# Kernel optimization log

Measured on AMD Instinct MI355X. Metric: run time of the kernel, lower is better.

The kernel has to match this reference:

```python
import jax, jax.numpy as jnp
import numpy as np

N, E, D, B, C = 50000, 800000, 128, 20000, 40
EPS_BN = 1e-3    # keras BatchNormalization default epsilon
EPS_NRM = 1e-12  # keras ops.nn.normalize epsilon
FFN_DIMS = {"pre": (D, D), "c1p": (D, D), "c1u": (2 * D, D), "c2p": (D, D), "c2u": (2 * D, D), "post": (D, D)}


def setup_inputs() -> dict:
    key = jax.random.key(0)
    ks = jax.random.split(key, 8)
    inp = {
        "node_features": jax.random.normal(ks[0], (N, D), jnp.float32),
        "edges": jax.random.randint(ks[1], (2, E), 0, N, dtype=jnp.int32),
        "edge_w": jax.random.uniform(ks[2], (E,), jnp.float32),
        "input_node_idx": jax.random.randint(ks[3], (B,), 0, N, dtype=jnp.int32),
    }
    for i, (name, (din, dout)) in enumerate(FFN_DIMS.items()):
        kw = jax.random.fold_in(key, 100 + i)
        inp[name + "_g"] = jnp.ones((din,), jnp.float32)
        inp[name + "_be"] = jnp.zeros((din,), jnp.float32)
        inp[name + "_mu"] = jnp.zeros((din,), jnp.float32)
        inp[name + "_var"] = jnp.ones((din,), jnp.float32)
        inp[name + "_w"] = jax.random.normal(kw, (din, dout), jnp.float32) * (1.0 / float(np.sqrt(din)))
        inp[name + "_bi"] = jnp.zeros((dout,), jnp.float32)
    inp["logits_w"] = jax.random.normal(ks[4], (D, C), jnp.float32) * (1.0 / float(np.sqrt(D)))
    inp["logits_b"] = jnp.zeros((C,), jnp.float32)
    return inp


def ffn(x, g, be, mu, var, w, bi):
    # BatchNorm (inference running stats) -> Dropout (identity) -> Dense + exact gelu
    xn = (x - mu) * jax.lax.rsqrt(var + EPS_BN) * g + be
    return jax.nn.gelu(xn @ w + bi, approximate=False)


def l2norm(x):
    n = jnp.sqrt(jnp.sum(x * x, axis=-1, keepdims=True))
    return x / jnp.maximum(n, EPS_NRM)


def graph_conv(x, node_idx, nbr_idx, ew, prep, upd):
    # gather neighbours -> prepare FFN -> edge-weighted -> segment_sum (reduce='sum')
    msgs = ffn(x[nbr_idx], *prep) * ew[:, None]                         # [E, D]
    red = jax.ops.segment_sum(msgs, node_idx, num_segments=x.shape[0])  # [N, D]
    h = jnp.concatenate([x, red], axis=1)                               # [N, 2D] (combination='concat')
    return l2norm(ffn(h, *upd))                                         # normalize=True


def reference(node_features, edges, edge_w, input_node_idx,
              pre_g, pre_be, pre_mu, pre_var, pre_w, pre_bi,
              c1p_g, c1p_be, c1p_mu, c1p_var, c1p_w, c1p_bi,
              c1u_g, c1u_be, c1u_mu, c1u_var, c1u_w, c1u_bi,
              c2p_g, c2p_be, c2p_mu, c2p_var, c2p_w, c2p_bi,
              c2u_g, c2u_be, c2u_mu, c2u_var, c2u_w, c2u_bi,
              post_g, post_be, post_mu, post_var, post_w, post_bi,
              logits_w, logits_b):
    ew = edge_w / jnp.sum(edge_w)                       # edge_W normalized at init
    node_idx, nbr_idx = edges[0], edges[1]
    x = ffn(node_features, pre_g, pre_be, pre_mu, pre_var, pre_w, pre_bi)
    x = graph_conv(x, node_idx, nbr_idx, ew,
                   (c1p_g, c1p_be, c1p_mu, c1p_var, c1p_w, c1p_bi),
                   (c1u_g, c1u_be, c1u_mu, c1u_var, c1u_w, c1u_bi)) + x
    x = graph_conv(x, node_idx, nbr_idx, ew,
                   (c2p_g, c2p_be, c2p_mu, c2p_var, c2p_w, c2p_bi),
                   (c2u_g, c2u_be, c2u_mu, c2u_var, c2u_w, c2u_bi)) + x
    x = ffn(x, post_g, post_be, post_mu, post_var, post_w, post_bi)
    return x[input_node_idx] @ logits_w + logits_b      # [B, C]
```

## Files before the change

### kernel.cpp

```cpp
#include <hip/hip_runtime.h>
#include <hip/hip_fp16.h>
#include <math.h>

static constexpr int D = 128;
static constexpr int CAP = 64;
static constexpr float EPS_BN = 1e-3f;

typedef short short8 __attribute__((ext_vector_type(8)));
typedef short short4v __attribute__((ext_vector_type(4)));
typedef float float4v __attribute__((ext_vector_type(4)));

__device__ __forceinline__ float gelu_exact(float x) {
    return 0.5f * x * (1.0f + erff(x * 0.70710678118654752f));
}

__device__ __forceinline__ void f32_to_hilo(float f, short& h, short& l) {
    unsigned u = __float_as_uint(f);
    h = (short)(u >> 16);
    float hf = __uint_as_float(u & 0xFFFF0000u);
    unsigned lu = __float_as_uint(f - hf);
    l = (short)(lu >> 16);
}

__device__ __forceinline__ short f32_to_bf16_rne(float f) {
    unsigned u = __float_as_uint(f);
    u += 0x7FFFu + ((u >> 16) & 1u);
    return (short)(u >> 16);
}

struct FoldArgs {
    const float* g[6]; const float* be[6]; const float* mu[6];
    const float* var[6]; const float* w[6]; const float* bi[6];
    short* wh[6]; short* wl[6]; float* bp[6]; int K[6];
};

__global__ void k_build(const int* __restrict__ edges, const float* __restrict__ ew,
                        int* __restrict__ cnt, float* __restrict__ sums,
                        unsigned* __restrict__ cw, FoldArgs fa, int E, int N, int fillBlocks) {
    __shared__ float sm[4];
    const int tid = threadIdx.x;
    const int lane = tid & 63, wvi = tid >> 6;

    if ((int)blockIdx.x < fillBlocks) {
        const int g = blockIdx.x & 7;
        const int bid = blockIdx.x >> 3;
        const int gstride = (fillBlocks >> 3) * 256;
        const int N8 = (N + 7) >> 3;
        const int lo = g * N8;
        const int hi = min(lo + N8, N);
        float s = 0.f;
        for (int e = bid * 256 + tid; e < E; e += gstride) {
            int dst = edges[e];
            if (dst >= lo && dst < hi) {
                int src = edges[E + e];
                float w = ew[e];
                s += w;
                unsigned short wb = __half_as_ushort(__float2half(w));
                int idx = atomicAdd(&cnt[dst], 1);
                if (idx < CAP)
                    cw[(size_t)dst * CAP + idx] = ((unsigned)src << 16) | (unsigned)wb;
            }
        }
        for (int off = 32; off > 0; off >>= 1) s += __shfl_down(s, off, 64);
        if (lane == 0) sm[wvi] = s;
        __syncthreads();
        if (tid == 0) {
            float t = sm[0] + sm[1] + sm[2] + sm[3];
            if (t != 0.f) atomicAdd(sums, t);
        }
    } else {
        const int idx = blockIdx.x - fillBlocks;
        const int f = idx >> 7;
        const int c = idx & 127;
        const int K = fa.K[f];
        const float* g = fa.g[f]; const float* be = fa.be[f];
        const float* mu = fa.mu[f]; const float* var = fa.var[f];
        const float* w = fa.w[f]; const float* bi = fa.bi[f];
        short* wh = fa.wh[f]; short* wl = fa.wl[f]; float* bp = fa.bp[f];
        float part = 0.f;
        for (int k = tid; k < K; k += blockDim.x) {
            float a = g[k] / sqrtf(var[k] + EPS_BN);
            float wv = w[k * D + c];
            float prod = a * wv;
            short hh, ll;
            f32_to_hilo(prod, hh, ll);
            wh[c * K + k] = hh;
            wl[c * K + k] = ll;
            part += (be[k] - mu[k] * a) * wv;
        }
        for (int off = 32; off > 0; off >>= 1) part += __shfl_down(part, off, 64);
        if (lane == 0) sm[wvi] = part;
        __syncthreads();
        if (tid == 0) bp[c] = bi[c] + sm[0] + sm[1] + sm[2] + sm[3];
    }
}

__global__ void k_reduce(const int* __restrict__ cnt, const unsigned* __restrict__ cw,
                         const float* __restrict__ sums, const __half* __restrict__ y,
                         float* __restrict__ red, int N) {
    int n = blockIdx.x * (blockDim.x >> 6) + (threadIdx.x >> 6);
    if (n >= N) return;
    float inv = 1.0f / sums[0];
    int lane = threadIdx.x & 63;
    int sub = lane >> 4;
    int q = lane & 15;
    int count = min(cnt[n], CAP);
    int start = n * CAP;
    int end = start + count;
    float acc[8] = {0.f, 0.f, 0.f, 0.f, 0.f, 0.f, 0.f, 0.f};
    int i = start + sub;
    if (i < end) {
        unsigned c = cw[i];
        for (;;) {
            int ni = i + 4;
            unsigned nc = 0;
            if (ni < end) nc = cw[ni];
            int src = (int)(c >> 16);
            float w = __half2float(__ushort_as_half((unsigned short)(c & 0xFFFFu))) * inv;
            float4 raw = *((const float4*)(y + (size_t)src * D) + q);
            const __half2* hp = (const __half2*)&raw;
            #pragma unroll
            for (int t = 0; t < 4; t++) {
                float2 f = __half22float2(hp[t]);
                acc[t * 2]     += w * f.x;
                acc[t * 2 + 1] += w * f.y;
            }
            if (ni >= end) break;
            i = ni; c = nc;
        }
    }
    #pragma unroll
    for (int t = 0; t < 8; t++) {
        acc[t] += __shfl_xor(acc[t], 16, 64);
        acc[t] += __shfl_xor(acc[t], 32, 64);
    }
    if (sub == 0) {
        float4 o0 = {acc[0], acc[1], acc[2], acc[3]};
        float4 o1 = {acc[4], acc[5], acc[6], acc[7]};
        *((float4*)(red + (size_t)n * D + q * 8)) = o0;
        *((float4*)(red + (size_t)n * D + q * 8 + 4)) = o1;
    }
}

template<int K, bool L2RES, bool OUT16, bool SPLIT3>
__device__ __forceinline__ void ffn_body(
    short (*__restrict__ Abuf)[128][72], short (*__restrict__ Wbuf)[128][72],
    float (*__restrict__ rs)[2],
    const float* __restrict__ A0, const float* __restrict__ A1,
    const short* __restrict__ Wh, const short* __restrict__ Wl,
    const float* __restrict__ bp, const float* __restrict__ resid,
    float* __restrict__ outf, __half* __restrict__ outh, int nrows)
{
    const int tid = threadIdx.x;
    const int lane = tid & 63;
    const int wv = tid >> 6;
    const int wr = wv >> 1;
    const int wc = wv & 1;
    const int m = lane & 15;
    const int quad = lane >> 4;
    const int rowBlock = blockIdx.x * 128;

    float4v acc[4][4];
    #pragma unroll
    for (int ti = 0; ti < 4; ti++)
        #pragma unroll
        for (int tj = 0; tj < 4; tj++)
            acc[ti][tj] = (float4v){0.f, 0.f, 0.f, 0.f};

    for (int cc = 0; cc < K / 64; cc++) {
        const float* Asrc = (K == 256 && cc >= 2) ? A1 : A0;
        const int kb = (K == 256) ? ((cc & 1) * 64) : (cc * 64);
        const int kw = cc * 64;

        #pragma unroll
        for (int t = 0; t < 8; t++) {
            int i = tid + t * 256;
            int r = i >> 4, k4 = i & 15;
            int grow = rowBlock + r; if (grow >= nrows) grow = nrows - 1;
            float4 f = *((const float4*)(Asrc + (size_t)grow * D + kb) + k4);
            if (SPLIT3) {
                short h0, l0, h1, l1, h2, l2, h3, l3;
                f32_to_hilo(f.x, h0, l0);
                f32_to_hilo(f.y, h1, l1);
                f32_to_hilo(f.z, h2, l2);
                f32_to_hilo(f.w, h3, l3);
                short4v hh = {h0, h1, h2, h3};
                short4v ll = {l0, l1, l2, l3};
                *(short4v*)&Abuf[0][r][k4 * 4] = hh;
                *(short4v*)&Abuf[1][r][k4 * 4] = ll;
            } else {
                short4v hh = {f32_to_bf16_rne(f.x), f32_to_bf16_rne(f.y),
                              f32_to_bf16_rne(f.z), f32_to_bf16_rne(f.w)};
                *(short4v*)&Abuf[0][r][k4 * 4] = hh;
            }
        }
        #pragma unroll
        for (int t = 0; t < 4; t++) {
            int i = tid + t * 256;
            int c = i >> 3, g = i & 7;
            short8 wh8 = *(const short8*)(Wh + (size_t)c * K + kw + g * 8);
            *(short8*)&Wbuf[0][c][g * 8] = wh8;
            if (SPLIT3) {
                short8 wl8 = *(const short8*)(Wl + (size_t)c * K + kw + g * 8);
                *(short8*)&Wbuf[1][c][g * 8] = wl8;
            }
        }
        __syncthreads();

        #pragma unroll
        for (int ks = 0; ks < 2; ks++) {
            short8 ah[4], bh[4];
            #pragma unroll
            for (int ti = 0; ti < 4; ti++)
                ah[ti] = *(const short8*)&Abuf[0][wr * 64 + ti * 16 + m][ks * 32 + quad * 8];
            #pragma unroll
            for (int tj = 0; tj < 4; tj++)
                bh[tj] = *(const short8*)&Wbuf[0][wc * 64 + tj * 16 + m][ks * 32 + quad * 8];
            if (SPLIT3) {
                short8 al[4], bl[4];
                #pragma unroll
                for (int ti = 0; ti < 4; ti++)
                    al[ti] = *(const short8*)&Abuf[1][wr * 64 + ti * 16 + m][ks * 32 + quad * 8];
                #pragma unroll
                for (int tj = 0; tj < 4; tj++)
                    bl[tj] = *(const short8*)&Wbuf[1][wc * 64 + tj * 16 + m][ks * 32 + quad * 8];
                #pragma unroll
                for (int ti = 0; ti < 4; ti++)
                    #pragma unroll
                    for (int tj = 0; tj < 4; tj++) {
                        acc[ti][tj] = __builtin_amdgcn_mfma_f32_16x16x32_bf16(al[ti], bh[tj], acc[ti][tj], 0, 0, 0);
                        acc[ti][tj] = __builtin_amdgcn_mfma_f32_16x16x32_bf16(ah[ti], bl[tj], acc[ti][tj], 0, 0, 0);
                        acc[ti][tj] = __builtin_amdgcn_mfma_f32_16x16x32_bf16(ah[ti], bh[tj], acc[ti][tj], 0, 0, 0);
                    }
            } else {
                #pragma unroll
                for (int ti = 0; ti < 4; ti++)
                    #pragma unroll
                    for (int tj = 0; tj < 4; tj++)
                        acc[ti][tj] = __builtin_amdgcn_mfma_f32_16x16x32_bf16(ah[ti], bh[tj], acc[ti][tj], 0, 0, 0);
            }
        }
        __syncthreads();
    }

    float bvv[4];
    #pragma unroll
    for (int tj = 0; tj < 4; tj++) bvv[tj] = bp[wc * 64 + tj * 16 + m];

    float g[4][4][4];
    #pragma unroll
    for (int ti = 0; ti < 4; ti++)
        #pragma unroll
        for (int tj = 0; tj < 4; tj++)
            #pragma unroll
            for (int r4 = 0; r4 < 4; r4++)
                g[ti][tj][r4] = gelu_exact(acc[ti][tj][r4] + bvv[tj]);

    if (L2RES) {
        #pragma unroll
        for (int ti = 0; ti < 4; ti++)
            #pragma unroll
            for (int r4 = 0; r4 < 4; r4++) {
                float ss = 0.f;
                #pragma unroll
                for (int tj = 0; tj < 4; tj++) ss += g[ti][tj][r4] * g[ti][tj][r4];
                ss += __shfl_xor(ss, 1, 64);
                ss += __shfl_xor(ss, 2, 64);
                ss += __shfl_xor(ss, 4, 64);
                ss += __shfl_xor(ss, 8, 64);
                if (m == 0) rs[wr * 64 + ti * 16 + quad * 4 + r4][wc] = ss;
            }
        __syncthreads();
        #pragma unroll
        for (int ti = 0; ti < 4; ti++)
            #pragma unroll
            for (int r4 = 0; r4 < 4; r4++) {
                int rib = wr * 64 + ti * 16 + quad * 4 + r4;
                float tot = rs[rib][0] + rs[rib][1];
                float inv = 1.0f / fmaxf(sqrtf(tot), 1e-12f);
                int row = rowBlock + rib;
                if (row < nrows) {
                    #pragma unroll
                    for (int tj = 0; tj < 4; tj++) {
                        int c = wc * 64 + tj * 16 + m;
                        outf[(size_t)row * D + c] = g[ti][tj][r4] * inv + resid[(size_t)row * D + c];
                    }
                }
            }
    } else {
        #pragma unroll
        for (int ti = 0; ti < 4; ti++)
            #pragma unroll
            for (int r4 = 0; r4 < 4; r4++) {
                int row = rowBlock + wr * 64 + ti * 16 + quad * 4 + r4;
                if (row < nrows) {
                    #pragma unroll
                    for (int tj = 0; tj < 4; tj++) {
                        int c = wc * 64 + tj * 16 + m;
                        if (OUT16) outh[(size_t)row * D + c] = __float2half(g[ti][tj][r4]);
                        else       outf[(size_t)row * D + c] = g[ti][tj][r4];
                    }
                }
            }
    }
}

__global__ __launch_bounds__(256, 2) void k_pair1(
    const float* __restrict__ nf,
    const short* __restrict__ Wh0, const short* __restrict__ Wl0, const float* __restrict__ Bp0,
    float* __restrict__ xA,
    const short* __restrict__ Wh1, const float* __restrict__ Bp1,
    __half* __restrict__ yh, int N)
{
    __shared__ short Abuf[2][128][72];
    __shared__ short Wbuf[2][128][72];
    __shared__ float rs[128][2];
    ffn_body<128, false, false, true>(Abuf, Wbuf, rs, nf, nullptr, Wh0, Wl0, Bp0, nullptr, xA, nullptr, N);
    __syncthreads();
    ffn_body<128, false, true, false>(Abuf, Wbuf, rs, xA, nullptr, Wh1, nullptr, Bp1, nullptr, nullptr, yh, N);
}

__global__ __launch_bounds__(256, 2) void k_pair2(
    const float* __restrict__ xA, const float* __restrict__ red,
    const short* __restrict__ Wh2, const short* __restrict__ Wl2, const float* __restrict__ Bp2,
    float* __restrict__ y,
    const short* __restrict__ Wh3, const float* __restrict__ Bp3,
    __half* __restrict__ yh, int N)
{
    __shared__ short Abuf[2][128][72];
    __shared__ short Wbuf[2][128][72];
    __shared__ float rs[128][2];
    ffn_body<256, true, false, true>(Abuf, Wbuf, rs, xA, red, Wh2, Wl2, Bp2, xA, y, nullptr, N);
    __syncthreads();
    ffn_body<128, false, true, false>(Abuf, Wbuf, rs, y, nullptr, Wh3, nullptr, Bp3, nullptr, nullptr, yh, N);
}

__global__ __launch_bounds__(256, 2) void k_pair3(
    const float* __restrict__ y, const float* __restrict__ red_in,
    const short* __restrict__ Wh4, const short* __restrict__ Wl4, const float* __restrict__ Bp4,
    float* __restrict__ xA,
    const short* __restrict__ Wh5, const short* __restrict__ Wl5, const float* __restrict__ Bp5,
    float* __restrict__ yout, int N)
{
    __shared__ short Abuf[2][128][72];
    __shared__ short Wbuf[2][128][72];
    __shared__ float rs[128][2];
    ffn_body<256, true, false, true>(Abuf, Wbuf, rs, y, red_in, Wh4, Wl4, Bp4, y, xA, nullptr, N);
    __syncthreads();
    ffn_body<128, false, false, true>(Abuf, Wbuf, rs, xA, nullptr, Wh5, Wl5, Bp5, nullptr, yout, nullptr, N);
}

__global__ void k_logits(const float* __restrict__ x, const int* __restrict__ idx,
                         const float* __restrict__ LW, const float* __restrict__ lb,
                         float* __restrict__ out, int B) {
    int wid = blockIdx.x * 4 + (threadIdx.x >> 6);
    int lane = threadIdx.x & 63;
    if (wid >= B) return;
    int row = __builtin_amdgcn_readfirstlane(idx[wid]);
    if (lane >= 40) return;
    float acc = lb[lane];
    const float4* xr = (const float4*)(x + (size_t)row * D);
    #pragma unroll 4
    for (int k4 = 0; k4 < 32; k4++) {
        float4 xv = xr[k4];
        acc += xv.x * LW[(4 * k4 + 0) * 40 + lane];
        acc += xv.y * LW[(4 * k4 + 1) * 40 + lane];
        acc += xv.z * LW[(4 * k4 + 2) * 40 + lane];
        acc += xv.w * LW[(4 * k4 + 3) * 40 + lane];
    }
    out[(size_t)wid * 40 + lane] = acc;
}

extern "C" void kernel_launch(void* const* d_in, const int* in_sizes, int n_in,
                              void* d_out, int out_size, void* d_ws, size_t ws_size,
                              hipStream_t stream) {
    const float* node_features = (const float*)d_in[0];
    const int*   edges         = (const int*)d_in[1];
    const float* edge_w        = (const float*)d_in[2];
    const int*   input_idx     = (const int*)d_in[3];
    const int N = in_sizes[0] / D;
    const int E = in_sizes[2];
    const int B = in_sizes[3];

    const float* P[6][6];
    for (int f = 0; f < 6; f++)
        for (int q = 0; q < 6; q++)
            P[f][q] = (const float*)d_in[4 + f * 6 + q];
    const float* logits_w = (const float*)d_in[40];
    const float* logits_b = (const float*)d_in[41];

    float* ws = (float*)d_ws;
    size_t nd = (size_t)N * D;
    float* xA  = ws;
    float* y   = ws + nd;
    float* red = ws + 2 * nd;
    float* p   = ws + 3 * nd;
    __half* yh = (__half*)p; p += nd / 2;
    const int Ks[6] = {128, 128, 256, 128, 256, 128};
    short* Wh[6]; short* Wl[6]; float* Bp[6];
    {
        short* sp = (short*)p;
        for (int f = 0; f < 6; f++) {
            Wh[f] = sp; sp += (size_t)Ks[f] * D;
            Wl[f] = sp; sp += (size_t)Ks[f] * D;
        }
        p = (float*)sp;
    }
    for (int f = 0; f < 6; f++) { Bp[f] = p; p += D; }
    int* cnt    = (int*)p; p += N;
    float* sums = p; p += 2;
    unsigned* cw = (unsigned*)p; p += (size_t)N * CAP;

    FoldArgs fa;
    for (int f = 0; f < 6; f++) {
        fa.g[f] = P[f][0]; fa.be[f] = P[f][1]; fa.mu[f] = P[f][2];
        fa.var[f] = P[f][3]; fa.w[f] = P[f][4]; fa.bi[f] = P[f][5];
        fa.wh[f] = Wh[f]; fa.wl[f] = Wl[f]; fa.bp[f] = Bp[f]; fa.K[f] = Ks[f];
    }

    const int fillBlocks = 1024;
    hipMemsetAsync(cnt, 0, ((size_t)N + 2) * sizeof(int), stream);
    k_build<<<fillBlocks + 768, 256, 0, stream>>>(edges, edge_w, cnt, sums, cw, fa, E, N, fillBlocks);

    const int gb = (N + 127) / 128;
    const int rb = (N + 3) / 4;

    k_pair1<<<gb, 256, 0, stream>>>(node_features, Wh[0], Wl[0], Bp[0], xA, Wh[1], Bp[1], yh, N);
    k_reduce<<<rb, 256, 0, stream>>>(cnt, cw, sums, yh, red, N);
    k_pair2<<<gb, 256, 0, stream>>>(xA, red, Wh[2], Wl[2], Bp[2], y, Wh[3], Bp[3], yh, N);
    k_reduce<<<rb, 256, 0, stream>>>(cnt, cw, sums, yh, red, N);
    k_pair3<<<gb, 256, 0, stream>>>(y, red, Wh[4], Wl[4], Bp[4], xA, Wh[5], Wl[5], Bp[5], red, N);
    k_logits<<<(B + 3) / 4, 256, 0, stream>>>(red, input_idx, logits_w, logits_b, (float*)d_out, B);
}
```

Before: 411.8 us.

## Fuse edge-bucket build into first FFN pair, store reductions in fp16, drop weight LDS staging

```diff
diff --git a/kernel.cpp b/kernel.cpp
--- a/kernel.cpp
+++ b/kernel.cpp
@@ -34,17 +34,229 @@
     short* wh[6]; short* wl[6]; float* bp[6]; int K[6];
 };
 
-__global__ void k_build(const int* __restrict__ edges, const float* __restrict__ ew,
-                        int* __restrict__ cnt, float* __restrict__ sums,
-                        unsigned* __restrict__ cw, FoldArgs fa, int E, int N, int fillBlocks) {
+__global__ void k_fold_all(FoldArgs fa) {
+    const int f = blockIdx.y;
+    const int c = blockIdx.x;
+    const int K = fa.K[f];
+    const float* g = fa.g[f]; const float* be = fa.be[f];
+    const float* mu = fa.mu[f]; const float* var = fa.var[f];
+    const float* w = fa.w[f]; const float* bi = fa.bi[f];
+    short* wh = fa.wh[f]; short* wl = fa.wl[f]; float* bp = fa.bp[f];
+    float part = 0.f;
+    for (int k = threadIdx.x; k < K; k += blockDim.x) {
+        float a = g[k] / sqrtf(var[k] + EPS_BN);
+        float wv = w[k * D + c];
+        float prod = a * wv;
+        short hh, ll;
+        f32_to_hilo(prod, hh, ll);
+        wh[c * K + k] = hh;
+        wl[c * K + k] = ll;
+        part += (be[k] - mu[k] * a) * wv;
+    }
+    for (int off = 32; off > 0; off >>= 1) part += __shfl_down(part, off, 64);
     __shared__ float sm[4];
+    int lane = threadIdx.x & 63, wv_ = threadIdx.x >> 6;
+    if (lane == 0) sm[wv_] = part;
+    __syncthreads();
+    if (threadIdx.x == 0) bp[c] = bi[c] + sm[0] + sm[1] + sm[2] + sm[3];
+}
+
+template<int K, bool L2RES, bool OUT16, bool SPLIT3>
+__device__ __forceinline__ void ffn_body(
+    short (*__restrict__ Abuf)[128][72], float (*__restrict__ rs)[2],
+    int rowBlock,
+    const float* __restrict__ A0, const __half* __restrict__ A1,
+    const float* __restrict__ sums,
+    const short* __restrict__ Wh, const short* __restrict__ Wl,
+    const float* __restrict__ bp, const float* __restrict__ resid,
+    float* __restrict__ outf, __half* __restrict__ outh, int nrows)
+{
     const int tid = threadIdx.x;
-    const int lane = tid & 63, wvi = tid >> 6;
-
-    if ((int)blockIdx.x < fillBlocks) {
+    const int lane = tid & 63;
+    const int wv = tid >> 6;
+    const int wr = wv >> 1;
+    const int wc = wv & 1;
+    const int m = lane & 15;
+    const int quad = lane >> 4;
+
+    float inv = 1.0f;
+    if (K == 256) inv = 1.0f / sums[0];
+
+    float4v acc[4][4];
+    #pragma unroll
+    for (int ti = 0; ti < 4; ti++)
+        #pragma unroll
+        for (int tj = 0; tj < 4; tj++)
+            acc[ti][tj] = (float4v){0.f, 0.f, 0.f, 0.f};
+
+    for (int cc = 0; cc < K / 64; cc++) {
+        const int kb = (K == 256) ? ((cc & 1) * 64) : (cc * 64);
+        const int kw = cc * 64;
+        const bool useA1 = (K == 256 && cc >= 2);
+
+        if (!useA1) {
+            #pragma unroll
+            for (int t = 0; t < 8; t++) {
+                int i = tid + t * 256;
+                int r = i >> 4, k4 = i & 15;
+                int grow = rowBlock + r; if (grow >= nrows) grow = nrows - 1;
+                float4 f = *((const float4*)(A0 + (size_t)grow * D + kb) + k4);
+                if (SPLIT3) {
+                    short h0, l0, h1, l1, h2, l2, h3, l3;
+                    f32_to_hilo(f.x, h0, l0);
+                    f32_to_hilo(f.y, h1, l1);
+                    f32_to_hilo(f.z, h2, l2);
+                    f32_to_hilo(f.w, h3, l3);
+                    short4v hh = {h0, h1, h2, h3};
+                    short4v ll = {l0, l1, l2, l3};
+                    *(short4v*)&Abuf[0][r][k4 * 4] = hh;
+                    *(short4v*)&Abuf[1][r][k4 * 4] = ll;
+                } else {
+                    short4v hh = {f32_to_bf16_rne(f.x), f32_to_bf16_rne(f.y),
+                                  f32_to_bf16_rne(f.z), f32_to_bf16_rne(f.w)};
+                    *(short4v*)&Abuf[0][r][k4 * 4] = hh;
+                }
+            }
+        } else {
+            #pragma unroll
+            for (int t = 0; t < 4; t++) {
+                int i = tid + t * 256;
+                int r = i >> 3, g8 = i & 7;
+                int grow = rowBlock + r; if (grow >= nrows) grow = nrows - 1;
+                float4 raw = *((const float4*)(A1 + (size_t)grow * D + kb) + g8);
+                const __half2* hp = (const __half2*)&raw;
+                short hs[8], ls[8];
+                #pragma unroll
+                for (int j = 0; j < 4; j++) {
+                    float2 fv = __half22float2(hp[j]);
+                    f32_to_hilo(fv.x * inv, hs[2 * j], ls[2 * j]);
+                    f32_to_hilo(fv.y * inv, hs[2 * j + 1], ls[2 * j + 1]);
+                }
+                short8 hv = {hs[0], hs[1], hs[2], hs[3], hs[4], hs[5], hs[6], hs[7]};
+                short8 lv = {ls[0], ls[1], ls[2], ls[3], ls[4], ls[5], ls[6], ls[7]};
+                *(short8*)&Abuf[0][r][g8 * 8] = hv;
+                *(short8*)&Abuf[1][r][g8 * 8] = lv;
+            }
+        }
+        __syncthreads();
+
+        #pragma unroll
+        for (int ks = 0; ks < 2; ks++) {
+            short8 ah[4], bh[4];
+            #pragma unroll
+            for (int ti = 0; ti < 4; ti++)
+                ah[ti] = *(const short8*)&Abuf[0][wr * 64 + ti * 16 + m][ks * 32 + quad * 8];
+            #pragma unroll
+            for (int tj = 0; tj < 4; tj++)
+                bh[tj] = *(const short8*)(Wh + (size_t)(wc * 64 + tj * 16 + m) * K + kw + ks * 32 + quad * 8);
+            if (SPLIT3) {
+                short8 al[4], bl[4];
+                #pragma unroll
+                for (int ti = 0; ti < 4; ti++)
+                    al[ti] = *(const short8*)&Abuf[1][wr * 64 + ti * 16 + m][ks * 32 + quad * 8];
+                #pragma unroll
+                for (int tj = 0; tj < 4; tj++)
+                    bl[tj] = *(const short8*)(Wl + (size_t)(wc * 64 + tj * 16 + m) * K + kw + ks * 32 + quad * 8);
+                #pragma unroll
+                for (int ti = 0; ti < 4; ti++)
+                    #pragma unroll
+                    for (int tj = 0; tj < 4; tj++) {
+                        acc[ti][tj] = __builtin_amdgcn_mfma_f32_16x16x32_bf16(al[ti], bh[tj], acc[ti][tj], 0, 0, 0);
+                        acc[ti][tj] = __builtin_amdgcn_mfma_f32_16x16x32_bf16(ah[ti], bl[tj], acc[ti][tj], 0, 0, 0);
+                        acc[ti][tj] = __builtin_amdgcn_mfma_f32_16x16x32_bf16(ah[ti], bh[tj], acc[ti][tj], 0, 0, 0);
+                    }
+            } else {
+                #pragma unroll
+                for (int ti = 0; ti < 4; ti++)
+                    #pragma unroll
+                    for (int tj = 0; tj < 4; tj++)
+                        acc[ti][tj] = __builtin_amdgcn_mfma_f32_16x16x32_bf16(ah[ti], bh[tj], acc[ti][tj], 0, 0, 0);
+            }
+        }
+        __syncthreads();
+    }
+
+    float bvv[4];
+    #pragma unroll
+    for (int tj = 0; tj < 4; tj++) bvv[tj] = bp[wc * 64 + tj * 16 + m];
+
+    float g[4][4][4];
+    #pragma unroll
+    for (int ti = 0; ti < 4; ti++)
+        #pragma unroll
+        for (int tj = 0; tj < 4; tj++)
+            #pragma unroll
+            for (int r4 = 0; r4 < 4; r4++)
+                g[ti][tj][r4] = gelu_exact(acc[ti][tj][r4] + bvv[tj]);
+
+    if (L2RES) {
+        #pragma unroll
+        for (int ti = 0; ti < 4; ti++)
+            #pragma unroll
+            for (int r4 = 0; r4 < 4; r4++) {
+                float ss = 0.f;
+                #pragma unroll
+                for (int tj = 0; tj < 4; tj++) ss += g[ti][tj][r4] * g[ti][tj][r4];
+                ss += __shfl_xor(ss, 1, 64);
+                ss += __shfl_xor(ss, 2, 64);
+                ss += __shfl_xor(ss, 4, 64);
+                ss += __shfl_xor(ss, 8, 64);
+                if (m == 0) rs[wr * 64 + ti * 16 + quad * 4 + r4][wc] = ss;
+            }
+        __syncthreads();
+        #pragma unroll
+        for (int ti = 0; ti < 4; ti++)
+            #pragma unroll
+            for (int r4 = 0; r4 < 4; r4++) {
+                int rib = wr * 64 + ti * 16 + quad * 4 + r4;
+                float tot = rs[rib][0] + rs[rib][1];
+                float invn = 1.0f / fmaxf(sqrtf(tot), 1e-12f);
+                int row = rowBlock + rib;
+                if (row < nrows) {
+                    #pragma unroll
+                    for (int tj = 0; tj < 4; tj++) {
+                        int c = wc * 64 + tj * 16 + m;
+                        outf[(size_t)row * D + c] = g[ti][tj][r4] * invn + resid[(size_t)row * D + c];
+                    }
+                }
+            }
+    } else {
+        #pragma unroll
+        for (int ti = 0; ti < 4; ti++)
+            #pragma unroll
+            for (int r4 = 0; r4 < 4; r4++) {
+                int row = rowBlock + wr * 64 + ti * 16 + quad * 4 + r4;
+                if (row < nrows) {
+                    #pragma unroll
+                    for (int tj = 0; tj < 4; tj++) {
+                        int c = wc * 64 + tj * 16 + m;
+                        if (OUT16) outh[(size_t)row * D + c] = __float2half(g[ti][tj][r4]);
+                        else       outf[(size_t)row * D + c] = g[ti][tj][r4];
+                    }
+                }
+            }
+    }
+}
+
+__global__ __launch_bounds__(256, 3) void k_pair1f(
+    const int* __restrict__ edges, const float* __restrict__ ew,
+    int* __restrict__ cnt, float* __restrict__ sums, unsigned* __restrict__ cw,
+    const float* __restrict__ nf,
+    const short* __restrict__ Wh0, const short* __restrict__ Wl0, const float* __restrict__ Bp0,
+    float* __restrict__ xA,
+    const short* __restrict__ Wh1, const float* __restrict__ Bp1,
+    __half* __restrict__ yh, int E, int N, int FB)
+{
+    __shared__ short Abuf[2][128][72];
+    __shared__ float rs[128][2];
+    __shared__ float sm4[4];
+
+    if ((int)blockIdx.x < FB) {
+        const int tid = threadIdx.x;
+        const int lane = tid & 63, wvi = tid >> 6;
         const int g = blockIdx.x & 7;
         const int bid = blockIdx.x >> 3;
-        const int gstride = (fillBlocks >> 3) * 256;
+        const int gstride = (FB >> 3) * 256;
         const int N8 = (N + 7) >> 3;
         const int lo = g * N8;
         const int hi = min(lo + N8, N);
@@ -62,45 +274,55 @@
             }
         }
         for (int off = 32; off > 0; off >>= 1) s += __shfl_down(s, off, 64);
-        if (lane == 0) sm[wvi] = s;
+        if (lane == 0) sm4[wvi] = s;
         __syncthreads();
         if (tid == 0) {
-            float t = sm[0] + sm[1] + sm[2] + sm[3];
+            float t = sm4[0] + sm4[1] + sm4[2] + sm4[3];
             if (t != 0.f) atomicAdd(sums, t);
         }
-    } else {
-        const int idx = blockIdx.x - fillBlocks;
-        const int f = idx >> 7;
-        const int c = idx & 127;
-        const int K = fa.K[f];
-        const float* g = fa.g[f]; const float* be = fa.be[f];
-        const float* mu = fa.mu[f]; const float* var = fa.var[f];
-        const float* w = fa.w[f]; const float* bi = fa.bi[f];
-        short* wh = fa.wh[f]; short* wl = fa.wl[f]; float* bp = fa.bp[f];
-        float part = 0.f;
-        for (int k = tid; k < K; k += blockDim.x) {
-            float a = g[k] / sqrtf(var[k] + EPS_BN);
-            float wv = w[k * D + c];
-            float prod = a * wv;
-            short hh, ll;
-            f32_to_hilo(prod, hh, ll);
-            wh[c * K + k] = hh;
-            wl[c * K + k] = ll;
-            part += (be[k] - mu[k] * a) * wv;
-        }
-        for (int off = 32; off > 0; off >>= 1) part += __shfl_down(part, off, 64);
-        if (lane == 0) sm[wvi] = part;
-        __syncthreads();
-        if (tid == 0) bp[c] = bi[c] + sm[0] + sm[1] + sm[2] + sm[3];
-    }
+        return;
+    }
+
+    int rowBlock = ((int)blockIdx.x - FB) * 128;
+    ffn_body<128, false, false, true>(Abuf, rs, rowBlock, nf, nullptr, nullptr, Wh0, Wl0, Bp0, nullptr, xA, nullptr, N);
+    __syncthreads();
+    ffn_body<128, false, true, false>(Abuf, rs, rowBlock, xA, nullptr, nullptr, Wh1, nullptr, Bp1, nullptr, nullptr, yh, N);
+}
+
+__global__ __launch_bounds__(256, 3) void k_pair2(
+    const float* __restrict__ xA, const __half* __restrict__ red, const float* __restrict__ sums,
+    const short* __restrict__ Wh2, const short* __restrict__ Wl2, const float* __restrict__ Bp2,
+    float* __restrict__ y,
+    const short* __restrict__ Wh3, const float* __restrict__ Bp3,
+    __half* __restrict__ yh, int N)
+{
+    __shared__ short Abuf[2][128][72];
+    __shared__ float rs[128][2];
+    int rowBlock = blockIdx.x * 128;
+    ffn_body<256, true, false, true>(Abuf, rs, rowBlock, xA, red, sums, Wh2, Wl2, Bp2, xA, y, nullptr, N);
+    __syncthreads();
+    ffn_body<128, false, true, false>(Abuf, rs, rowBlock, y, nullptr, nullptr, Wh3, nullptr, Bp3, nullptr, nullptr, yh, N);
+}
+
+__global__ __launch_bounds__(256, 3) void k_pair3(
+    const float* __restrict__ y, const __half* __restrict__ red, const float* __restrict__ sums,
+    const short* __restrict__ Wh4, const short* __restrict__ Wl4, const float* __restrict__ Bp4,
+    float* __restrict__ xA,
+    const short* __restrict__ Wh5, const short* __restrict__ Wl5, const float* __restrict__ Bp5,
+    __half* __restrict__ yh, int N)
+{
+    __shared__ short Abuf[2][128][72];
+    __shared__ float rs[128][2];
+    int rowBlock = blockIdx.x * 128;
+    ffn_body<256, true, false, true>(Abuf, rs, rowBlock, y, red, sums, Wh4, Wl4, Bp4, y, xA, nullptr, N);
+    __syncthreads();
+    ffn_body<128, false, true, true>(Abuf, rs, rowBlock, xA, nullptr, nullptr, Wh5, Wl5, Bp5, nullptr, nullptr, yh, N);
 }
 
 __global__ void k_reduce(const int* __restrict__ cnt, const unsigned* __restrict__ cw,
-                         const float* __restrict__ sums, const __half* __restrict__ y,
-                         float* __restrict__ red, int N) {
+                         const __half* __restrict__ y, __half* __restrict__ red, int N) {
     int n = blockIdx.x * (blockDim.x >> 6) + (threadIdx.x >> 6);
     if (n >= N) return;
-    float inv = 1.0f / sums[0];
     int lane = threadIdx.x & 63;
     int sub = lane >> 4;
     int q = lane & 15;
@@ -116,7 +338,7 @@
             unsigned nc = 0;
             if (ni < end) nc = cw[ni];
             int src = (int)(c >> 16);
-            float w = __half2float(__ushort_as_half((unsigned short)(c & 0xFFFFu))) * inv;
+            float w = __half2float(__ushort_as_half((unsigned short)(c & 0xFFFFu)));
             float4 raw = *((const float4*)(y + (size_t)src * D) + q);
             const __half2* hp = (const __half2*)&raw;
             #pragma unroll
@@ -135,222 +357,16 @@
         acc[t] += __shfl_xor(acc[t], 32, 64);
     }
     if (sub == 0) {
-        float4 o0 = {acc[0], acc[1], acc[2], acc[3]};
-        float4 o1 = {acc[4], acc[5], acc[6], acc[7]};
-        *((float4*)(red + (size_t)n * D + q * 8)) = o0;
-        *((float4*)(red + (size_t)n * D + q * 8 + 4)) = o1;
-    }
-}
-
-template<int K, bool L2RES, bool OUT16, bool SPLIT3>
-__device__ __forceinline__ void ffn_body(
-    short (*__restrict__ Abuf)[128][72], short (*__restrict__ Wbuf)[128][72],
-    float (*__restrict__ rs)[2],
-    const float* __restrict__ A0, const float* __restrict__ A1,
-    const short* __restrict__ Wh, const short* __restrict__ Wl,
-    const float* __restrict__ bp, const float* __restrict__ resid,
-    float* __restrict__ outf, __half* __restrict__ outh, int nrows)
-{
-    const int tid = threadIdx.x;
-    const int lane = tid & 63;
-    const int wv = tid >> 6;
-    const int wr = wv >> 1;
-    const int wc = wv & 1;
-    const int m = lane & 15;
-    const int quad = lane >> 4;
-    const int rowBlock = blockIdx.x * 128;
-
-    float4v acc[4][4];
-    #pragma unroll
-    for (int ti = 0; ti < 4; ti++)
-        #pragma unroll
-        for (int tj = 0; tj < 4; tj++)
-            acc[ti][tj] = (float4v){0.f, 0.f, 0.f, 0.f};
-
-    for (int cc = 0; cc < K / 64; cc++) {
-        const float* Asrc = (K == 256 && cc >= 2) ? A1 : A0;
-        const int kb = (K == 256) ? ((cc & 1) * 64) : (cc * 64);
-        const int kw = cc * 64;
-
-        #pragma unroll
-        for (int t = 0; t < 8; t++) {
-            int i = tid + t * 256;
-            int r = i >> 4, k4 = i & 15;
-            int grow = rowBlock + r; if (grow >= nrows) grow = nrows - 1;
-            float4 f = *((const float4*)(Asrc + (size_t)grow * D + kb) + k4);
-            if (SPLIT3) {
-                short h0, l0, h1, l1, h2, l2, h3, l3;
-                f32_to_hilo(f.x, h0, l0);
-                f32_to_hilo(f.y, h1, l1);
-                f32_to_hilo(f.z, h2, l2);
-                f32_to_hilo(f.w, h3, l3);
-                short4v hh = {h0, h1, h2, h3};
-                short4v ll = {l0, l1, l2, l3};
-                *(short4v*)&Abuf[0][r][k4 * 4] = hh;
-                *(short4v*)&Abuf[1][r][k4 * 4] = ll;
-            } else {
-                short4v hh = {f32_to_bf16_rne(f.x), f32_to_bf16_rne(f.y),
-                              f32_to_bf16_rne(f.z), f32_to_bf16_rne(f.w)};
-                *(short4v*)&Abuf[0][r][k4 * 4] = hh;
-            }
-        }
-        #pragma unroll
-        for (int t = 0; t < 4; t++) {
-            int i = tid + t * 256;
-            int c = i >> 3, g = i & 7;
-            short8 wh8 = *(const short8*)(Wh + (size_t)c * K + kw + g * 8);
-            *(short8*)&Wbuf[0][c][g * 8] = wh8;
-            if (SPLIT3) {
-                short8 wl8 = *(const short8*)(Wl + (size_t)c * K + kw + g * 8);
-                *(short8*)&Wbuf[1][c][g * 8] = wl8;
-            }
-        }
-        __syncthreads();
-
-        #pragma unroll
-        for (int ks = 0; ks < 2; ks++) {
-            short8 ah[4], bh[4];
-            #pragma unroll
-            for (int ti = 0; ti < 4; ti++)
-                ah[ti] = *(const short8*)&Abuf[0][wr * 64 + ti * 16 + m][ks * 32 + quad * 8];
-            #pragma unroll
-            for (int tj = 0; tj < 4; tj++)
-                bh[tj] = *(const short8*)&Wbuf[0][wc * 64 + tj * 16 + m][ks * 32 + quad * 8];
-            if (SPLIT3) {
-                short8 al[4], bl[4];
-                #pragma unroll
-                for (int ti = 0; ti < 4; ti++)
-                    al[ti] = *(const short8*)&Abuf[1][wr * 64 + ti * 16 + m][ks * 32 + quad * 8];
-                #pragma unroll
-                for (int tj = 0; tj < 4; tj++)
-                    bl[tj] = *(const short8*)&Wbuf[1][wc * 64 + tj * 16 + m][ks * 32 + quad * 8];
-                #pragma unroll
-                for (int ti = 0; ti < 4; ti++)
-                    #pragma unroll
-                    for (int tj = 0; tj < 4; tj++) {
-                        acc[ti][tj] = __builtin_amdgcn_mfma_f32_16x16x32_bf16(al[ti], bh[tj], acc[ti][tj], 0, 0, 0);
-                        acc[ti][tj] = __builtin_amdgcn_mfma_f32_16x16x32_bf16(ah[ti], bl[tj], acc[ti][tj], 0, 0, 0);
-                        acc[ti][tj] = __builtin_amdgcn_mfma_f32_16x16x32_bf16(ah[ti], bh[tj], acc[ti][tj], 0, 0, 0);
-                    }
-            } else {
-                #pragma unroll
-                for (int ti = 0; ti < 4; ti++)
-                    #pragma unroll
-                    for (int tj = 0; tj < 4; tj++)
-                        acc[ti][tj] = __builtin_amdgcn_mfma_f32_16x16x32_bf16(ah[ti], bh[tj], acc[ti][tj], 0, 0, 0);
-            }
-        }
-        __syncthreads();
-    }
-
-    float bvv[4];
-    #pragma unroll
-    for (int tj = 0; tj < 4; tj++) bvv[tj] = bp[wc * 64 + tj * 16 + m];
-
-    float g[4][4][4];
-    #pragma unroll
-    for (int ti = 0; ti < 4; ti++)
-        #pragma unroll
-        for (int tj = 0; tj < 4; tj++)
-            #pragma unroll
-            for (int r4 = 0; r4 < 4; r4++)
-                g[ti][tj][r4] = gelu_exact(acc[ti][tj][r4] + bvv[tj]);
-
-    if (L2RES) {
-        #pragma unroll
-        for (int ti = 0; ti < 4; ti++)
-            #pragma unroll
-            for (int r4 = 0; r4 < 4; r4++) {
-                float ss = 0.f;
-                #pragma unroll
-                for (int tj = 0; tj < 4; tj++) ss += g[ti][tj][r4] * g[ti][tj][r4];
-                ss += __shfl_xor(ss, 1, 64);
-                ss += __shfl_xor(ss, 2, 64);
-                ss += __shfl_xor(ss, 4, 64);
-                ss += __shfl_xor(ss, 8, 64);
-                if (m == 0) rs[wr * 64 + ti * 16 + quad * 4 + r4][wc] = ss;
-            }
-        __syncthreads();
-        #pragma unroll
-        for (int ti = 0; ti < 4; ti++)
-            #pragma unroll
-            for (int r4 = 0; r4 < 4; r4++) {
-                int rib = wr * 64 + ti * 16 + quad * 4 + r4;
-                float tot = rs[rib][0] + rs[rib][1];
-                float inv = 1.0f / fmaxf(sqrtf(tot), 1e-12f);
-                int row = rowBlock + rib;
-                if (row < nrows) {
-                    #pragma unroll
-                    for (int tj = 0; tj < 4; tj++) {
-                        int c = wc * 64 + tj * 16 + m;
-                        outf[(size_t)row * D + c] = g[ti][tj][r4] * inv + resid[(size_t)row * D + c];
-                    }
-                }
-            }
-    } else {
-        #pragma unroll
-        for (int ti = 0; ti < 4; ti++)
-            #pragma unroll
-            for (int r4 = 0; r4 < 4; r4++) {
-                int row = rowBlock + wr * 64 + ti * 16 + quad * 4 + r4;
-                if (row < nrows) {
-                    #pragma unroll
-                    for (int tj = 0; tj < 4; tj++) {
-                        int c = wc * 64 + tj * 16 + m;
-                        if (OUT16) outh[(size_t)row * D + c] = __float2half(g[ti][tj][r4]);
-                        else       outf[(size_t)row * D + c] = g[ti][tj][r4];
-                    }
-                }
-            }
-    }
-}
-
-__global__ __launch_bounds__(256, 2) void k_pair1(
-    const float* __restrict__ nf,
-    const short* __restrict__ Wh0, const short* __restrict__ Wl0, const float* __restrict__ Bp0,
-    float* __restrict__ xA,
-    const short* __restrict__ Wh1, const float* __restrict__ Bp1,
-    __half* __restrict__ yh, int N)
-{
-    __shared__ short Abuf[2][128][72];
-    __shared__ short Wbuf[2][128][72];
-    __shared__ float rs[128][2];
-    ffn_body<128, false, false, true>(Abuf, Wbuf, rs, nf, nullptr, Wh0, Wl0, Bp0, nullptr, xA, nullptr, N);
-    __syncthreads();
-    ffn_body<128, false, true, false>(Abuf, Wbuf, rs, xA, nullptr, Wh1, nullptr, Bp1, nullptr, nullptr, yh, N);
-}
-
-__global__ __launch_bounds__(256, 2) void k_pair2(
-    const float* __restrict__ xA, const float* __restrict__ red,
-    const short* __restrict__ Wh2, const short* __restrict__ Wl2, const float* __restrict__ Bp2,
-    float* __restrict__ y,
-    const short* __restrict__ Wh3, const float* __restrict__ Bp3,
-    __half* __restrict__ yh, int N)
-{
-    __shared__ short Abuf[2][128][72];
-    __shared__ short Wbuf[2][128][72];
-    __shared__ float rs[128][2];
-    ffn_body<256, true, false, true>(Abuf, Wbuf, rs, xA, red, Wh2, Wl2, Bp2, xA, y, nullptr, N);
-    __syncthreads();
-    ffn_body<128, false, true, false>(Abuf, Wbuf, rs, y, nullptr, Wh3, nullptr, Bp3, nullptr, nullptr, yh, N);
-}
-
-__global__ __launch_bounds__(256, 2) void k_pair3(
-    const float* __restrict__ y, const float* __restrict__ red_in,
-    const short* __restrict__ Wh4, const short* __restrict__ Wl4, const float* __restrict__ Bp4,
-    float* __restrict__ xA,
-    const short* __restrict__ Wh5, const short* __restrict__ Wl5, const float* __restrict__ Bp5,
-    float* __restrict__ yout, int N)
-{
-    __shared__ short Abuf[2][128][72];
-    __shared__ short Wbuf[2][128][72];
-    __shared__ float rs[128][2];
-    ffn_body<256, true, false, true>(Abuf, Wbuf, rs, y, red_in, Wh4, Wl4, Bp4, y, xA, nullptr, N);
-    __syncthreads();
-    ffn_body<128, false, false, true>(Abuf, Wbuf, rs, xA, nullptr, Wh5, Wl5, Bp5, nullptr, yout, nullptr, N);
-}
-
-__global__ void k_logits(const float* __restrict__ x, const int* __restrict__ idx,
+        float4 ov;
+        __half2* op = (__half2*)&ov;
+        #pragma unroll
+        for (int t = 0; t < 4; t++)
+            op[t] = __floats2half2_rn(acc[t * 2], acc[t * 2 + 1]);
+        *((float4*)(red + (size_t)n * D + q * 8)) = ov;
+    }
+}
+
+__global__ void k_logits(const __half* __restrict__ x, const int* __restrict__ idx,
                          const float* __restrict__ LW, const float* __restrict__ lb,
                          float* __restrict__ out, int B) {
     int wid = blockIdx.x * 4 + (threadIdx.x >> 6);
@@ -361,12 +377,15 @@
     float acc = lb[lane];
     const float4* xr = (const float4*)(x + (size_t)row * D);
     #pragma unroll 4
-    for (int k4 = 0; k4 < 32; k4++) {
-        float4 xv = xr[k4];
-        acc += xv.x * LW[(4 * k4 + 0) * 40 + lane];
-        acc += xv.y * LW[(4 * k4 + 1) * 40 + lane];
-        acc += xv.z * LW[(4 * k4 + 2) * 40 + lane];
-        acc += xv.w * LW[(4 * k4 + 3) * 40 + lane];
+    for (int k8 = 0; k8 < 16; k8++) {
+        float4 raw = xr[k8];
+        const __half2* hp = (const __half2*)&raw;
+        #pragma unroll
+        for (int j = 0; j < 4; j++) {
+            float2 f = __half22float2(hp[j]);
+            acc += f.x * LW[(k8 * 8 + 2 * j) * 40 + lane];
+            acc += f.y * LW[(k8 * 8 + 2 * j + 1) * 40 + lane];
+        }
     }
     out[(size_t)wid * 40 + lane] = acc;
 }
@@ -393,9 +412,9 @@
     size_t nd = (size_t)N * D;
     float* xA  = ws;
     float* y   = ws + nd;
-    float* red = ws + 2 * nd;
-    float* p   = ws + 3 * nd;
-    __half* yh = (__half*)p; p += nd / 2;
+    float* p   = ws + 2 * nd;
+    __half* redh = (__half*)p; p += nd / 2;
+    __half* yh   = (__half*)p; p += nd / 2;
     const int Ks[6] = {128, 128, 256, 128, 256, 128};
     short* Wh[6]; short* Wl[6]; float* Bp[6];
     {
@@ -418,17 +437,18 @@
         fa.wh[f] = Wh[f]; fa.wl[f] = Wl[f]; fa.bp[f] = Bp[f]; fa.K[f] = Ks[f];
     }
 
-    const int fillBlocks = 1024;
-    hipMemsetAsync(cnt, 0, ((size_t)N + 2) * sizeof(int), stream);
-    k_build<<<fillBlocks + 768, 256, 0, stream>>>(edges, edge_w, cnt, sums, cw, fa, E, N, fillBlocks);
-
     const int gb = (N + 127) / 128;
     const int rb = (N + 3) / 4;
-
-    k_pair1<<<gb, 256, 0, stream>>>(node_features, Wh[0], Wl[0], Bp[0], xA, Wh[1], Bp[1], yh, N);
-    k_reduce<<<rb, 256, 0, stream>>>(cnt, cw, sums, yh, red, N);
-    k_pair2<<<gb, 256, 0, stream>>>(xA, red, Wh[2], Wl[2], Bp[2], y, Wh[3], Bp[3], yh, N);
-    k_reduce<<<rb, 256, 0, stream>>>(cnt, cw, sums, yh, red, N);
-    k_pair3<<<gb, 256, 0, stream>>>(y, red, Wh[4], Wl[4], Bp[4], xA, Wh[5], Wl[5], Bp[5], red, N);
-    k_logits<<<(B + 3) / 4, 256, 0, stream>>>(red, input_idx, logits_w, logits_b, (float*)d_out, B);
-}
+    const int FB = 1024;
+
+    hipMemsetAsync(cnt, 0, ((size_t)N + 2) * sizeof(int), stream);
+    k_fold_all<<<dim3(D, 6), 256, 0, stream>>>(fa);
+    k_pair1f<<<FB + gb, 256, 0, stream>>>(edges, edge_w, cnt, sums, cw,
+                                          node_features, Wh[0], Wl[0], Bp[0], xA,
+                                          Wh[1], Bp[1], yh, E, N, FB);
+    k_reduce<<<rb, 256, 0, stream>>>(cnt, cw, yh, redh, N);
+    k_pair2<<<gb, 256, 0, stream>>>(xA, redh, sums, Wh[2], Wl[2], Bp[2], y, Wh[3], Bp[3], yh, N);
+    k_reduce<<<rb, 256, 0, stream>>>(cnt, cw, yh, redh, N);
+    k_pair3<<<gb, 256, 0, stream>>>(y, redh, sums, Wh[4], Wl[4], Bp[4], xA, Wh[5], Wl[5], Bp[5], yh, N);
+    k_logits<<<(B + 3) / 4, 256, 0, stream>>>(yh, input_idx, logits_w, logits_b, (float*)d_out, B);
+}
```

After: 520.9 us. 26.5% more time.
